# Performance work log

Hardware: AMD Instinct MI355X
Metric: run time of the kernel (lower is better)

The kernel has to match this reference:

```python
import jax, jax.numpy as jnp
import numpy as np

EPS = 1e-12  # torch F.normalize eps


def conv1x1(x, W, b):
    # x: [B,C,H,W], W: [O,C], b: [O]
    return jnp.einsum('bchw,oc->bohw', x, W) + b[None, :, None, None]


def l2norm(x):
    n = jnp.linalg.norm(x, axis=-1, keepdims=True)
    return x / jnp.maximum(n, EPS)


def setup_inputs() -> dict:
    key = jax.random.key(0)
    ks = jax.random.split(key, 12)
    B, C, H, W = 8, 192, 128, 128
    heads = 8
    s = 1.0 / np.sqrt(C)
    return {
        'x1': jax.random.normal(ks[0], (B, C, H, W), jnp.float32),
        'x2': jax.random.normal(ks[1], (B, C, H, W), jnp.float32),
        'W_proj': jax.random.normal(ks[2], (C, C), jnp.float32) * s,
        'b_proj': jax.random.normal(ks[3], (C,), jnp.float32) * 0.01,
        'gate': jnp.ones((1,), jnp.float32),
        'pos_bias_h': jax.random.normal(ks[4], (1, heads, 1, 1), jnp.float32) * 0.01,
        'pos_bias_w': jax.random.normal(ks[5], (1, heads, 1, 1), jnp.float32) * 0.01,
        'W_m1': jax.random.normal(ks[6], (C, C), jnp.float32) * s,
        'b_m1': jax.random.normal(ks[7], (C,), jnp.float32) * 0.01,
        'W_m2': jax.random.normal(ks[8], (C, C), jnp.float32) * s,
        'b_m2': jax.random.normal(ks[9], (C,), jnp.float32) * 0.01,
    }


def reference(x1, x2, W_proj, b_proj, gate, pos_bias_h, pos_bias_w, W_m1, b_m1, W_m2, b_m2):
    temperature = 0.01
    num_heads = pos_bias_h.shape[1]
    B, C, h, w = x1.shape
    c = C // num_heads

    out1 = conv1x1(x1, W_proj, b_proj)
    out2 = conv1x1(x2, W_proj, b_proj)

    def to_h_tokens(o):  # 'b (head c) h w -> b head h (w c)'
        return o.reshape(B, num_heads, c, h, w).transpose(0, 1, 3, 4, 2).reshape(B, num_heads, h, w * c)

    def to_w_tokens(o):  # 'b (head c) h w -> b head w (h c)'
        return o.reshape(B, num_heads, c, h, w).transpose(0, 1, 4, 3, 2).reshape(B, num_heads, w, h * c)

    k1 = to_h_tokens(out1)
    v1 = k1
    k2 = to_w_tokens(out2)
    v2 = k2
    q2 = to_w_tokens(out1)
    q1 = to_h_tokens(out2)

    q1 = l2norm(q1); q2 = l2norm(q2)
    k1 = l2norm(k1); k2 = l2norm(k2)

    attn1 = jnp.einsum('bnid,bnjd->bnij', q1, k1) / temperature + pos_bias_h
    attn2 = jnp.einsum('bnid,bnjd->bnij', q2, k2) / temperature + pos_bias_w
    attn1 = jax.nn.softmax(attn1, axis=-1)
    attn2 = jax.nn.softmax(attn2, axis=-1)

    out3 = jnp.einsum('bnij,bnjd->bnid', attn1, v1) + q1  # [B,heads,h,w*c]
    out4 = jnp.einsum('bnij,bnjd->bnid', attn2, v2) + q2  # [B,heads,w,h*c]

    # 'b head h (w c) -> b (head c) h w'
    out3 = out3.reshape(B, num_heads, h, w, c).transpose(0, 1, 4, 2, 3).reshape(B, C, h, w)
    # 'b head w (h c) -> b (head c) h w'
    out4 = out4.reshape(B, num_heads, w, h, c).transpose(0, 1, 4, 3, 2).reshape(B, C, h, w)

    g = jax.nn.sigmoid(gate)[0]
    fusion = g * out3 + (1.0 - g) * out4
    out = conv1x1(fusion, W_proj, b_proj)
    out = conv1x1(jax.nn.gelu(conv1x1(out, W_m1, b_m1), approximate=False), W_m2, b_m2) + x1 + x2
    return out
```

## Files before the change

kernel.cpp:

```cpp
#include <hip/hip_runtime.h>
#include <math.h>


#define N_PIX 16384
#define W_DIM 128
#define C_DIM 192
#define C_PH  24
#define ELEMS 25165824
#define TINV  100.0f

typedef __bf16 bf16x8 __attribute__((ext_vector_type(8)));
typedef float  f32x4  __attribute__((ext_vector_type(4)));

__device__ __forceinline__ unsigned short f2bf(float f) {
    union { float f; unsigned u; } x; x.f = f;
    unsigned r = x.u + 0x7FFF + ((x.u >> 16) & 1);
    return (unsigned short)(r >> 16);
}
__device__ __forceinline__ float bf2f(unsigned short h) {
    union { unsigned u; float f; } x; x.u = ((unsigned)h) << 16; return x.f;
}
__device__ __forceinline__ unsigned pack2(unsigned short a, unsigned short b) {
    return (unsigned)a | ((unsigned)b << 16);
}

__global__ __launch_bounds__(256)
void conv_f32in(const float* __restrict__ X, const float* __restrict__ Wt,
                const float* __restrict__ bias, unsigned short* __restrict__ Y)
{
    __shared__ unsigned short Ah[64][40];
    __shared__ unsigned short Bh[256][40];

    const int tid = threadIdx.x;
    const int p0 = blockIdx.x << 8;
    const int m0 = blockIdx.y << 6;
    const int b  = blockIdx.z;
    const float* Xb = X + (size_t)b * C_DIM * N_PIX;

    const int wave = tid >> 6, lane = tid & 63;
    const int quad = lane >> 4, l16 = lane & 15;
    const int mw = (wave & 1) << 5;
    const int nw = (wave >> 1) << 7;
    const int koff = quad << 3;

    f32x4 acc[2][8];
    #pragma unroll
    for (int i = 0; i < 2; ++i)
        #pragma unroll
        for (int j = 0; j < 8; ++j) acc[i][j] = (f32x4){0.f, 0.f, 0.f, 0.f};

    for (int k0 = 0; k0 < C_DIM; k0 += 32) {
        #pragma unroll
        for (int i = 0; i < 2; ++i) {
            const int a = (tid << 1) + i;
            const int m = a >> 3, kq = a & 7;
            const float4 v = *(const float4*)(Wt + (size_t)(m0 + m) * C_DIM + k0 + (kq << 2));
            uint2 pk; pk.x = pack2(f2bf(v.x), f2bf(v.y)); pk.y = pack2(f2bf(v.z), f2bf(v.w));
            *(uint2*)(&Ah[m][kq << 2]) = pk;
        }
        #pragma unroll
        for (int r = 0; r < 2; ++r) {
            const int u = tid + (r << 8);
            const int kq = u & 7, p4 = (u >> 3) << 2;
            float4 f[4];
            #pragma unroll
            for (int i = 0; i < 4; ++i)
                f[i] = *(const float4*)(Xb + (size_t)(k0 + (kq << 2) + i) * N_PIX + p0 + p4);
            #pragma unroll
            for (int j = 0; j < 4; ++j) {
                uint2 pk;
                pk.x = pack2(f2bf((&f[0].x)[j]), f2bf((&f[1].x)[j]));
                pk.y = pack2(f2bf((&f[2].x)[j]), f2bf((&f[3].x)[j]));
                *(uint2*)(&Bh[p4 + j][kq << 2]) = pk;
            }
        }
        __syncthreads();

        bf16x8 af[2];
        #pragma unroll
        for (int mf = 0; mf < 2; ++mf)
            af[mf] = *(const bf16x8*)(&Ah[mw + (mf << 4) + l16][koff]);
        #pragma unroll
        for (int nf = 0; nf < 8; ++nf) {
            const bf16x8 bfr = *(const bf16x8*)(&Bh[nw + (nf << 4) + l16][koff]);
            #pragma unroll
            for (int mf = 0; mf < 2; ++mf)
                acc[mf][nf] = __builtin_amdgcn_mfma_f32_16x16x32_bf16(af[mf], bfr, acc[mf][nf], 0, 0, 0);
        }
        __syncthreads();
    }

    const size_t outb = (size_t)b * C_DIM * N_PIX;
    #pragma unroll
    for (int mf = 0; mf < 2; ++mf) {
        #pragma unroll
        for (int r = 0; r < 4; ++r) {
            const int m = m0 + mw + (mf << 4) + (quad << 2) + r;
            const float bm = bias[m];
            const size_t row = outb + (size_t)m * N_PIX;
            #pragma unroll
            for (int nf = 0; nf < 8; ++nf) {
                const int p = p0 + nw + (nf << 4) + l16;
                Y[row + p] = f2bf(acc[mf][nf][r] + bm);
            }
        }
    }
}

template<int MODE>
__global__ __launch_bounds__(256)
void conv_b16in(const unsigned short* __restrict__ X, const float* __restrict__ Wt,
                const float* __restrict__ bias, void* __restrict__ Yv,
                const float* __restrict__ R1, const float* __restrict__ R2)
{
    __shared__ unsigned short Ah[64][40];
    __shared__ unsigned short Bh[256][40];

    const int tid = threadIdx.x;
    const int p0 = blockIdx.x << 8;
    const int m0 = blockIdx.y << 6;
    const int b  = blockIdx.z;
    const unsigned short* Xb = X + (size_t)b * C_DIM * N_PIX;

    const int wave = tid >> 6, lane = tid & 63;
    const int quad = lane >> 4, l16 = lane & 15;
    const int mw = (wave & 1) << 5;
    const int nw = (wave >> 1) << 7;
    const int koff = quad << 3;

    f32x4 acc[2][8];
    #pragma unroll
    for (int i = 0; i < 2; ++i)
        #pragma unroll
        for (int j = 0; j < 8; ++j) acc[i][j] = (f32x4){0.f, 0.f, 0.f, 0.f};

    for (int k0 = 0; k0 < C_DIM; k0 += 32) {
        #pragma unroll
        for (int i = 0; i < 2; ++i) {
            const int a = (tid << 1) + i;
            const int m = a >> 3, kq = a & 7;
            const float4 v = *(const float4*)(Wt + (size_t)(m0 + m) * C_DIM + k0 + (kq << 2));
            uint2 pk; pk.x = pack2(f2bf(v.x), f2bf(v.y)); pk.y = pack2(f2bf(v.z), f2bf(v.w));
            *(uint2*)(&Ah[m][kq << 2]) = pk;
        }
        {
            const int kq = tid & 7, pg = (tid >> 3) << 3;
            uint4 f[4];
            #pragma unroll
            for (int i = 0; i < 4; ++i)
                f[i] = *(const uint4*)(Xb + (size_t)(k0 + (kq << 2) + i) * N_PIX + p0 + pg);
            #pragma unroll
            for (int j = 0; j < 8; ++j) {
                const unsigned short e0 = ((const unsigned short*)&f[0])[j];
                const unsigned short e1 = ((const unsigned short*)&f[1])[j];
                const unsigned short e2 = ((const unsigned short*)&f[2])[j];
                const unsigned short e3 = ((const unsigned short*)&f[3])[j];
                uint2 pk; pk.x = pack2(e0, e1); pk.y = pack2(e2, e3);
                *(uint2*)(&Bh[pg + j][kq << 2]) = pk;
            }
        }
        __syncthreads();

        bf16x8 af[2];
        #pragma unroll
        for (int mf = 0; mf < 2; ++mf)
            af[mf] = *(const bf16x8*)(&Ah[mw + (mf << 4) + l16][koff]);
        #pragma unroll
        for (int nf = 0; nf < 8; ++nf) {
            const bf16x8 bfr = *(const bf16x8*)(&Bh[nw + (nf << 4) + l16][koff]);
            #pragma unroll
            for (int mf = 0; mf < 2; ++mf)
                acc[mf][nf] = __builtin_amdgcn_mfma_f32_16x16x32_bf16(af[mf], bfr, acc[mf][nf], 0, 0, 0);
        }
        __syncthreads();
    }

    const size_t outb = (size_t)b * C_DIM * N_PIX;
    #pragma unroll
    for (int mf = 0; mf < 2; ++mf) {
        #pragma unroll
        for (int r = 0; r < 4; ++r) {
            const int m = m0 + mw + (mf << 4) + (quad << 2) + r;
            const float bm = bias[m];
            const size_t row = outb + (size_t)m * N_PIX;
            #pragma unroll
            for (int nf = 0; nf < 8; ++nf) {
                const int p = p0 + nw + (nf << 4) + l16;
                float v = acc[mf][nf][r] + bm;
                if (MODE == 1) v = 0.5f * v * (1.0f + erff(v * 0.70710678118654752f));
                if (MODE == 2) {
                    v += R1[row + p] + R2[row + p];
                    ((float*)Yv)[row + p] = v;
                } else {
                    ((unsigned short*)Yv)[row + p] = f2bf(v);
                }
            }
        }
    }
}

__global__ __launch_bounds__(256)
void transpose_norms(const unsigned short* __restrict__ o1,
                     const unsigned short* __restrict__ o2,
                     unsigned short* __restrict__ o1T,
                     unsigned short* __restrict__ o2T,
                     float* __restrict__ norms)
{
    __shared__ float hs[128];
    __shared__ float wss[128];

    const int tid = threadIdx.x;
    const int ch  = blockIdx.x;
    const int b   = blockIdx.y;
    const int src = blockIdx.z;
    const int n   = ch / 24;

    const size_t poff = ((size_t)b * C_DIM + ch) * N_PIX;
    const unsigned short* pin = (src ? o2 : o1) + poff;
    unsigned short* pout      = (src ? o2T : o1T) + poff;

    if (tid >= 128) wss[tid - 128] = 0.0f;
    __syncthreads();

    const int h0 = (tid >> 4) << 3;
    const int w0 = (tid & 15) << 3;

    uint4 r[8];
    #pragma unroll
    for (int i = 0; i < 8; ++i)
        r[i] = *(const uint4*)(pin + (size_t)(h0 + i) * W_DIM + w0);

    #pragma unroll
    for (int j = 0; j < 8; ++j) {
        uint4 o;
        unsigned short* op = (unsigned short*)&o;
        #pragma unroll
        for (int i = 0; i < 8; ++i)
            op[i] = ((const unsigned short*)&r[i])[j];
        *(uint4*)(pout + (size_t)(w0 + j) * W_DIM + h0) = o;
    }

    float hp[8], wp[8];
    #pragma unroll
    for (int i = 0; i < 8; ++i) { hp[i] = 0.0f; wp[i] = 0.0f; }
    #pragma unroll
    for (int i = 0; i < 8; ++i) {
        #pragma unroll
        for (int j = 0; j < 8; ++j) {
            const float v = bf2f(((const unsigned short*)&r[i])[j]);
            hp[i] += v * v;
            wp[j] += v * v;
        }
    }
    #pragma unroll
    for (int i = 0; i < 8; ++i) {
        #pragma unroll
        for (int off = 1; off < 16; off <<= 1) hp[i] += __shfl_xor(hp[i], off);
    }
    const int l16 = tid & 15;
    if (l16 < 8) hs[h0 + l16] = hp[l16];
    #pragma unroll
    for (int j = 0; j < 8; ++j) {
        wp[j] += __shfl_xor(wp[j], 16);
        wp[j] += __shfl_xor(wp[j], 32);
    }
    if ((tid & 63) < 16) {
        #pragma unroll
        for (int j = 0; j < 8; ++j) atomicAdd(&wss[w0 + j], wp[j]);
    }
    __syncthreads();

    float* np_ = norms + ((size_t)(src * 8 + b) * 8 + n) * 256;
    if (tid < 128) atomicAdd(&np_[tid], hs[tid]);
    else           atomicAdd(&np_[tid], wss[tid - 128]);
}

__global__ __launch_bounds__(1024)
void scores_softmax(const unsigned short* __restrict__ o1,
                    const unsigned short* __restrict__ o2,
                    const unsigned short* __restrict__ o1T,
                    const unsigned short* __restrict__ o2T,
                    const float* __restrict__ norms, const float* __restrict__ gate,
                    unsigned short* __restrict__ P)
{
    __shared__ float Sred[3][4][16][132];
    __shared__ float rqv[64], rkv[128];

    const int tid = threadIdx.x;
    const int i0  = blockIdx.x << 6;
    const int bn  = blockIdx.y;
    const int dir = blockIdx.z;
    const int b = bn >> 3, n = bn & 7;

    const size_t base = (size_t)b * C_DIM * N_PIX + (size_t)n * C_PH * N_PIX;
    const unsigned short* Qb = (dir == 0 ? o2 : o1T) + base;
    const unsigned short* Kb = (dir == 0 ? o1 : o2T) + base;

    const int qsrc = (dir == 0) ? 1 : 0;
    const float* qn_g = norms + ((size_t)(qsrc * 8 + b) * 8 + n) * 256 + dir * 128;
    const float* kn_g = norms + ((size_t)((1 - qsrc) * 8 + b) * 8 + n) * 256 + dir * 128;

    if (tid < 64)        rqv[tid]      = TINV * rsqrtf(fmaxf(qn_g[i0 + tid], 1e-24f));
    else if (tid < 192)  rkv[tid - 64] = rsqrtf(fmaxf(kn_g[tid - 64], 1e-24f));

    const int wave = tid >> 6, lane = tid & 63;
    const int iw = wave & 3;
    const int kw = wave >> 2;
    const int quad = lane >> 4, l16 = lane & 15;

    const unsigned short* rq = Qb + (size_t)(i0 + (iw << 4) + l16) * W_DIM + (quad << 3);
    const unsigned short* rk = Kb + (size_t)l16 * W_DIM + (quad << 3);

    f32x4 acc[8];
    #pragma unroll
    for (int j = 0; j < 8; ++j) acc[j] = (f32x4){0.f, 0.f, 0.f, 0.f};

    #pragma unroll 2
    for (int s = 0; s < 24; ++s) {
        const int ks = kw * 24 + s;
        const size_t off = (size_t)(ks >> 2) * N_PIX + (size_t)((ks & 3) << 5);
        const uint4 qf = *(const uint4*)(rq + off);
        uint4 kf[8];
        #pragma unroll
        for (int nf = 0; nf < 8; ++nf)
            kf[nf] = *(const uint4*)(rk + off + (nf << 11));
        const bf16x8 a = *(const bf16x8*)&qf;
        #pragma unroll
        for (int nf = 0; nf < 8; ++nf)
            acc[nf] = __builtin_amdgcn_mfma_f32_16x16x32_bf16(a, *(const bf16x8*)&kf[nf], acc[nf], 0, 0, 0);
    }

    if (kw != 0) {
        float* dst = &Sred[kw - 1][iw][0][0];
        #pragma unroll
        for (int nf = 0; nf < 8; ++nf)
            #pragma unroll
            for (int r = 0; r < 4; ++r)
                dst[(size_t)((quad << 2) + r) * 132 + (nf << 4) + l16] = acc[nf][r];
    }
    __syncthreads();
    if (kw != 0) return;

    const float g = 1.0f / (1.0f + __expf(-gate[0]));
    const float gs = (dir == 0) ? g : (1.0f - g);
    unsigned short* Pg = P + (((size_t)dir * 64 + bn) << 14);

    #pragma unroll
    for (int r = 0; r < 4; ++r) {
        const int row16 = (quad << 2) + r;
        const int i_loc = (iw << 4) + row16;
        const float rqs = rqv[i_loc];
        float v[8], m = -1e30f;
        #pragma unroll
        for (int nf = 0; nf < 8; ++nf) {
            const int col = (nf << 4) + l16;
            float sv = acc[nf][r]
                     + Sred[0][iw][row16][col]
                     + Sred[1][iw][row16][col]
                     + Sred[2][iw][row16][col];
            v[nf] = sv * rqs * rkv[col];
            m = fmaxf(m, v[nf]);
        }
        #pragma unroll
        for (int off = 1; off < 16; off <<= 1) m = fmaxf(m, __shfl_xor(m, off));
        float s = 0.0f;
        #pragma unroll
        for (int nf = 0; nf < 8; ++nf) { v[nf] = __expf(v[nf] - m); s += v[nf]; }
        #pragma unroll
        for (int off = 1; off < 16; off <<= 1) s += __shfl_xor(s, off);
        const float inv = gs / s;
        const size_t rowo = (size_t)(i0 + i_loc) * 128;
        #pragma unroll
        for (int nf = 0; nf < 8; ++nf)
            Pg[rowo + (nf << 4) + l16] = f2bf(v[nf] * inv);
    }
}

__global__ __launch_bounds__(256)
void pv_mfma(const unsigned short* __restrict__ o1, const unsigned short* __restrict__ o2,
             const unsigned short* __restrict__ o1T,
             const unsigned short* __restrict__ P, const float* __restrict__ norms,
             const float* __restrict__ gate, unsigned short* __restrict__ fusion)
{
    __shared__ unsigned short P1s[128][40];
    __shared__ unsigned short A2s[128][40];
    __shared__ unsigned short P2s[128][40];
    __shared__ unsigned short A1Ts[128][40];
    __shared__ float rqs[256];

    const int tid = threadIdx.x;
    const int ch  = blockIdx.x;
    const int bn  = blockIdx.y;
    const int b = bn >> 3, n = bn & 7;

    const size_t pbase = (size_t)b * C_DIM * N_PIX + ((size_t)n * C_PH + ch) * N_PIX;
    const unsigned short* A1  = o1 + pbase;
    const unsigned short* A2  = o2 + pbase;
    const unsigned short* A1T = o1T + pbase;
    const unsigned short* P1 = P + ((size_t)bn << 14);
    const unsigned short* P2 = P + ((size_t)(64 + bn) << 14);
    unsigned short* Fp = fusion + pbase;

    const float g = 1.0f / (1.0f + __expf(-gate[0]));
    if (tid < 128)
        rqs[tid] = g * rsqrtf(fmaxf(norms[(((size_t)8 + b) * 8 + n) * 256 + tid], 1e-24f));
    else
        rqs[tid] = (1.0f - g) * rsqrtf(fmaxf(norms[(((size_t)b) * 8 + n) * 256 + 128 + (tid - 128)], 1e-24f));

    const int wave = tid >> 6, lane = tid & 63;
    const int quad = lane >> 4, l16 = lane & 15;
    const int i0w = wave << 5;
    const int koff = quad << 3;

    f32x4 acc[2][8];
    #pragma unroll
    for (int i = 0; i < 2; ++i)
        #pragma unroll
        for (int j = 0; j < 8; ++j) acc[i][j] = (f32x4){0.f, 0.f, 0.f, 0.f};

    for (int k0 = 0; k0 < 128; k0 += 32) {
        #pragma unroll
        for (int r = 0; r < 2; ++r) {
            const int u = tid + (r << 8);
            const int row = u >> 2, k8 = u & 3;
            const size_t go = (size_t)row * 128 + k0 + (k8 << 3);
            *(uint4*)(&P1s[row][k8 << 3])  = *(const uint4*)(P1 + go);
            *(uint4*)(&A2s[row][k8 << 3])  = *(const uint4*)(A2 + go);
            *(uint4*)(&P2s[row][k8 << 3])  = *(const uint4*)(P2 + go);
            *(uint4*)(&A1Ts[row][k8 << 3]) = *(const uint4*)(A1T + go);
        }
        __syncthreads();

        bf16x8 p1f[2], a2f[2];
        #pragma unroll
        for (int mf = 0; mf < 2; ++mf) {
            p1f[mf] = *(const bf16x8*)(&P1s[i0w + (mf << 4) + l16][koff]);
            a2f[mf] = *(const bf16x8*)(&A2s[i0w + (mf << 4) + l16][koff]);
        }
        #pragma unroll
        for (int nf = 0; nf < 8; ++nf) {
            const bf16x8 b1 = *(const bf16x8*)(&A1Ts[(nf << 4) + l16][koff]);
            const bf16x8 b2 = *(const bf16x8*)(&P2s[(nf << 4) + l16][koff]);
            #pragma unroll
            for (int mf = 0; mf < 2; ++mf) {
                acc[mf][nf] = __builtin_amdgcn_mfma_f32_16x16x32_bf16(p1f[mf], b1, acc[mf][nf], 0, 0, 0);
                acc[mf][nf] = __builtin_amdgcn_mfma_f32_16x16x32_bf16(a2f[mf], b2, acc[mf][nf], 0, 0, 0);
            }
        }
        __syncthreads();
    }

    #pragma unroll
    for (int mf = 0; mf < 2; ++mf) {
        #pragma unroll
        for (int r = 0; r < 4; ++r) {
            const int i = i0w + (mf << 4) + (quad << 2) + r;
            const float c1 = rqs[i];
            #pragma unroll
            for (int nf = 0; nf < 8; ++nf) {
                const int w = (nf << 4) + l16;
                const size_t o = (size_t)i * 128 + w;
                const float F = acc[mf][nf][r] + c1 * bf2f(A2[o]) + rqs[128 + w] * bf2f(A1[o]);
                Fp[o] = f2bf(F);
            }
        }
    }
}

extern "C" void kernel_launch(void* const* d_in, const int* in_sizes, int n_in,
                              void* d_out, int out_size, void* d_ws, size_t ws_size,
                              hipStream_t stream)
{
    (void)in_sizes; (void)n_in; (void)out_size; (void)ws_size;
    const float* x1     = (const float*)d_in[0];
    const float* x2     = (const float*)d_in[1];
    const float* W_proj = (const float*)d_in[2];
    const float* b_proj = (const float*)d_in[3];
    const float* gate   = (const float*)d_in[4];
    const float* W_m1   = (const float*)d_in[7];
    const float* b_m1   = (const float*)d_in[8];
    const float* W_m2   = (const float*)d_in[9];
    const float* b_m2   = (const float*)d_in[10];

    unsigned short* o1    = (unsigned short*)d_ws;
    unsigned short* o2    = o1 + ELEMS;
    float*          norms = (float*)(o2 + ELEMS);
    unsigned short* Pbuf  = (unsigned short*)(norms + 32768);

    unsigned short* o2T    = (unsigned short*)d_out;
    unsigned short* fusion = o2T;
    unsigned short* o1T    = o2T + ELEMS;

    const dim3 cgrid(64, 3, 8);
    conv_f32in<<<cgrid, 256, 0, stream>>>(x1, W_proj, b_proj, o1);
    conv_f32in<<<cgrid, 256, 0, stream>>>(x2, W_proj, b_proj, o2);

    hipMemsetAsync(norms, 0, 32768 * sizeof(float), stream);
    transpose_norms<<<dim3(192, 8, 2), 256, 0, stream>>>(o1, o2, o1T, o2T, norms);

    scores_softmax<<<dim3(2, 64, 2), 1024, 0, stream>>>(o1, o2, o1T, o2T, norms, gate, Pbuf);
    pv_mfma<<<dim3(24, 64), 256, 0, stream>>>(o1, o2, o1T, Pbuf, norms, gate, fusion);

    conv_b16in<0><<<cgrid, 256, 0, stream>>>(fusion, W_proj, b_proj, o1, nullptr, nullptr);
    conv_b16in<1><<<cgrid, 256, 0, stream>>>(o1, W_m1, b_m1, o2, nullptr, nullptr);
    conv_b16in<2><<<cgrid, 256, 0, stream>>>(o2, W_m2, b_m2, d_out, x1, x2);
}
```

Measured before the change: 635.3 us.

## Stage score-kernel Q/K tiles through LDS with register prefetch, drop split-K waves

```diff
diff --git a/kernel.cpp b/kernel.cpp
--- a/kernel.cpp
+++ b/kernel.cpp
@@ -275,7 +275,10 @@
     else           atomicAdd(&np_[tid], wss[tid - 128]);
 }
 
-__global__ __launch_bounds__(1024)
+#define SS_KBASE 17408
+#define SS_STRIDE 272
+
+__global__ __launch_bounds__(256)
 void scores_softmax(const unsigned short* __restrict__ o1,
                     const unsigned short* __restrict__ o2,
                     const unsigned short* __restrict__ o1T,
@@ -283,12 +286,12 @@
                     const float* __restrict__ norms, const float* __restrict__ gate,
                     unsigned short* __restrict__ P)
 {
-    __shared__ float Sred[3][4][16][132];
+    __shared__ __align__(16) unsigned char SMEM[SS_KBASE + 128 * SS_STRIDE];
     __shared__ float rqv[64], rkv[128];
 
     const int tid = threadIdx.x;
-    const int i0  = blockIdx.x << 6;
-    const int bn  = blockIdx.y;
+    const int bn  = blockIdx.x;
+    const int i0  = blockIdx.y << 6;
     const int dir = blockIdx.z;
     const int b = bn >> 3, n = bn & 7;
 
@@ -304,42 +307,74 @@
     else if (tid < 192)  rkv[tid - 64] = rsqrtf(fmaxf(kn_g[tid - 64], 1e-24f));
 
     const int wave = tid >> 6, lane = tid & 63;
-    const int iw = wave & 3;
-    const int kw = wave >> 2;
     const int quad = lane >> 4, l16 = lane & 15;
 
-    const unsigned short* rq = Qb + (size_t)(i0 + (iw << 4) + l16) * W_DIM + (quad << 3);
-    const unsigned short* rk = Kb + (size_t)l16 * W_DIM + (quad << 3);
+    const char* qsrc0 = (const char*)(Qb + (size_t)i0 * W_DIM) + tid * 16;
+    const char* ksrc0 = (const char*)Kb + tid * 16;
+    const int l_base = ((tid >> 4) * SS_STRIDE) + ((tid & 15) << 4);
 
     f32x4 acc[8];
     #pragma unroll
     for (int j = 0; j < 8; ++j) acc[j] = (f32x4){0.f, 0.f, 0.f, 0.f};
 
-    #pragma unroll 2
+    uint4 rg[12];
+
+#define SS_ISSUE(sch) do { \
+        const char* qs_ = qsrc0 + (size_t)(sch) * 32768; \
+        const char* ks_ = ksrc0 + (size_t)(sch) * 32768; \
+        _Pragma("unroll") \
+        for (int j_ = 0; j_ < 4; ++j_) { \
+            const char* p_ = qs_ + j_ * 4096; \
+            asm volatile("global_load_dwordx4 %0, %1, off" : "=v"(rg[j_]) : "v"(p_)); \
+        } \
+        _Pragma("unroll") \
+        for (int j_ = 0; j_ < 8; ++j_) { \
+            const char* p_ = ks_ + j_ * 4096; \
+            asm volatile("global_load_dwordx4 %0, %1, off" : "=v"(rg[4 + j_]) : "v"(p_)); \
+        } \
+        __builtin_amdgcn_sched_barrier(0); \
+    } while (0)
+
+#define SS_WRITE() do { \
+        asm volatile("s_waitcnt vmcnt(0)" ::: "memory"); \
+        __builtin_amdgcn_sched_barrier(0); \
+        _Pragma("unroll") \
+        for (int j_ = 0; j_ < 4; ++j_) \
+            *(uint4*)(SMEM + j_ * 4352 + l_base) = rg[j_]; \
+        _Pragma("unroll") \
+        for (int j_ = 0; j_ < 8; ++j_) \
+            *(uint4*)(SMEM + SS_KBASE + j_ * 4352 + l_base) = rg[4 + j_]; \
+    } while (0)
+
+#define SS_COMPUTE() do { \
+        _Pragma("unroll") \
+        for (int ks_ = 0; ks_ < 4; ++ks_) { \
+            const int ko_ = ks_ * 64 + quad * 16; \
+            const bf16x8 a_ = *(const bf16x8*)(SMEM + ((wave << 4) + l16) * SS_STRIDE + ko_); \
+            _Pragma("unroll") \
+            for (int nf_ = 0; nf_ < 8; ++nf_) { \
+                const bf16x8 b_ = *(const bf16x8*)(SMEM + SS_KBASE + ((nf_ << 4) + l16) * SS_STRIDE + ko_); \
+                acc[nf_] = __builtin_amdgcn_mfma_f32_16x16x32_bf16(a_, b_, acc[nf_], 0, 0, 0); \
+            } \
+        } \
+    } while (0)
+
+    SS_ISSUE(0);
+    SS_WRITE();
+    __syncthreads();
+    #pragma unroll 1
     for (int s = 0; s < 24; ++s) {
-        const int ks = kw * 24 + s;
-        const size_t off = (size_t)(ks >> 2) * N_PIX + (size_t)((ks & 3) << 5);
-        const uint4 qf = *(const uint4*)(rq + off);
-        uint4 kf[8];
-        #pragma unroll
-        for (int nf = 0; nf < 8; ++nf)
-            kf[nf] = *(const uint4*)(rk + off + (nf << 11));
-        const bf16x8 a = *(const bf16x8*)&qf;
-        #pragma unroll
-        for (int nf = 0; nf < 8; ++nf)
-            acc[nf] = __builtin_amdgcn_mfma_f32_16x16x32_bf16(a, *(const bf16x8*)&kf[nf], acc[nf], 0, 0, 0);
-    }
-
-    if (kw != 0) {
-        float* dst = &Sred[kw - 1][iw][0][0];
-        #pragma unroll
-        for (int nf = 0; nf < 8; ++nf)
-            #pragma unroll
-            for (int r = 0; r < 4; ++r)
-                dst[(size_t)((quad << 2) + r) * 132 + (nf << 4) + l16] = acc[nf][r];
-    }
-    __syncthreads();
-    if (kw != 0) return;
+        if (s + 1 < 24) SS_ISSUE(s + 1);
+        SS_COMPUTE();
+        __syncthreads();
+        if (s + 1 < 24) {
+            SS_WRITE();
+            __syncthreads();
+        }
+    }
+#undef SS_ISSUE
+#undef SS_WRITE
+#undef SS_COMPUTE
 
     const float g = 1.0f / (1.0f + __expf(-gate[0]));
     const float gs = (dir == 0) ? g : (1.0f - g);
@@ -347,18 +382,12 @@
 
     #pragma unroll
     for (int r = 0; r < 4; ++r) {
-        const int row16 = (quad << 2) + r;
-        const int i_loc = (iw << 4) + row16;
+        const int i_loc = (wave << 4) + (quad << 2) + r;
         const float rqs = rqv[i_loc];
         float v[8], m = -1e30f;
         #pragma unroll
         for (int nf = 0; nf < 8; ++nf) {
-            const int col = (nf << 4) + l16;
-            float sv = acc[nf][r]
-                     + Sred[0][iw][row16][col]
-                     + Sred[1][iw][row16][col]
-                     + Sred[2][iw][row16][col];
-            v[nf] = sv * rqs * rkv[col];
+            v[nf] = acc[nf][r] * rqs * rkv[(nf << 4) + l16];
             m = fmaxf(m, v[nf]);
         }
         #pragma unroll
@@ -498,7 +527,7 @@
     hipMemsetAsync(norms, 0, 32768 * sizeof(float), stream);
     transpose_norms<<<dim3(192, 8, 2), 256, 0, stream>>>(o1, o2, o1T, o2T, norms);
 
-    scores_softmax<<<dim3(2, 64, 2), 1024, 0, stream>>>(o1, o2, o1T, o2T, norms, gate, Pbuf);
+    scores_softmax<<<dim3(64, 2, 2), 256, 0, stream>>>(o1, o2, o1T, o2T, norms, gate, Pbuf);
     pv_mfma<<<dim3(24, 64), 256, 0, stream>>>(o1, o2, o1T, Pbuf, norms, gate, fusion);
 
     conv_b16in<0><<<cgrid, 256, 0, stream>>>(fusion, W_proj, b_proj, o1, nullptr, nullptr);
```

Measured after the change: 580.5 us. -8.6%, faster.
